# Kernel optimization log

Measured on AMD Instinct MI355X. Metric: run time of the kernel, lower is better.

The kernel has to match this reference:

```python
import jax, jax.numpy as jnp
import numpy as np

TOP_K = 2

def setup_inputs() -> dict:
    key = jax.random.key(0)
    ks = jax.random.split(key, 6)
    B, L, D, E = 4, 4096, 1024, 8
    s = 1.0 / np.sqrt(D)
    return {
        "x": jax.random.normal(ks[0], (B, L, D), dtype=jnp.float32),
        "Wr": jax.random.normal(ks[1], (E, D), dtype=jnp.float32) * s,
        "W1": jax.random.normal(ks[2], (E, D, D), dtype=jnp.float32) * s,
        "b1": jax.random.normal(ks[3], (E, D), dtype=jnp.float32) * 0.01,
        "W2": jax.random.normal(ks[4], (E, D, D), dtype=jnp.float32) * s,
        "b2": jax.random.normal(ks[5], (E, D), dtype=jnp.float32) * 0.01,
    }

def reference(x, Wr, W1, b1, W2, b2):
    # x: [B,L,D]; Wr: [E,D]; W1/W2: [E,D,D]; b1/b2: [E,D]
    E = Wr.shape[0]
    logits = jnp.einsum("bld,ed->ble", x, Wr)           # router, no bias
    probs = jax.nn.softmax(logits, axis=-1)
    topw, topi = jax.lax.top_k(probs, TOP_K)             # [B,L,K]
    topw = topw / jnp.sum(topw, axis=-1, keepdims=True)  # renormalize
    # combine weights per expert: [B,L,E], zero where expert not selected
    comb = jnp.sum(jax.nn.one_hot(topi, E, dtype=x.dtype) * topw[..., None], axis=-2)
    out = jnp.zeros_like(x)
    for e in range(E):  # small fixed expert count
        h = jax.nn.gelu(jnp.einsum("bld,fd->blf", x, W1[e]) + b1[e], approximate=False)
        y = jnp.einsum("blf,df->bld", h, W2[e]) + b2[e]
        out = out + comb[..., e:e + 1] * y
    return out
```

## Files before the change

### kernel.cpp

```cpp
#include <hip/hip_runtime.h>
#include <hip/hip_bf16.h>
#include <cstdint>
#include <cstddef>

#define NTOK 16384
#define DDIM 1024
#define NEXP 8
#define CPAD 32

typedef __attribute__((ext_vector_type(8))) short bf16x8;
typedef __attribute__((ext_vector_type(4))) float f32x4;

__device__ __forceinline__ unsigned short f2bf(float f) {
  union { float f; unsigned u; } c; c.f = f;
  unsigned r = (c.u + 0x7FFFu + ((c.u >> 16) & 1u)) >> 16;
  return (unsigned short)r;
}

__device__ __forceinline__ float gelu_exact(float v) {
  return 0.5f * v * (1.0f + erff(v * 0.70710678118654752440f));
}

#define GL2LDS(gp, lp) __builtin_amdgcn_global_load_lds( \
    (__attribute__((address_space(1))) void*)(gp),       \
    (__attribute__((address_space(3))) void*)(lp), 16, 0, 0)

__global__ void cast_k(const float* __restrict__ src, unsigned short* __restrict__ dst, int n4) {
  int i = blockIdx.x * blockDim.x + threadIdx.x;
  if (i >= n4) return;
  float4 a = ((const float4*)src)[i];
  union { unsigned short s[4]; uint2 v; } o;
  o.s[0] = f2bf(a.x); o.s[1] = f2bf(a.y); o.s[2] = f2bf(a.z); o.s[3] = f2bf(a.w);
  ((uint2*)dst)[i] = o.v;
}

__global__ __launch_bounds__(256)
void castx_router_k(const float* __restrict__ x, const float* __restrict__ Wr,
                    unsigned short* __restrict__ xb, int* __restrict__ tokE,
                    float2* __restrict__ tokW) {
  const int t = blockIdx.x;
  const int tid = threadIdx.x;
  const int w = tid >> 6, lane = tid & 63;

  float4 xv = ((const float4*)x)[(size_t)t * 256 + tid];
  union { unsigned short s[4]; uint2 v; } o;
  o.s[0] = f2bf(xv.x); o.s[1] = f2bf(xv.y); o.s[2] = f2bf(xv.z); o.s[3] = f2bf(xv.w);
  ((uint2*)xb)[(size_t)t * 256 + tid] = o.v;

  const float4* Wr4 = (const float4*)Wr;
  float p[NEXP];
#pragma unroll
  for (int e = 0; e < NEXP; ++e) {
    float4 wv = Wr4[e * 256 + tid];
    p[e] = xv.x * wv.x + xv.y * wv.y + xv.z * wv.z + xv.w * wv.w;
  }
#pragma unroll
  for (int e = 0; e < NEXP; ++e) {
    float v = p[e];
#pragma unroll
    for (int off = 32; off >= 1; off >>= 1) v += __shfl_xor(v, off, 64);
    p[e] = v;
  }
  __shared__ float red[4][NEXP];
  if (lane == 0) {
#pragma unroll
    for (int e = 0; e < NEXP; ++e) red[w][e] = p[e];
  }
  __syncthreads();
  if (tid == 0) {
    float s[NEXP];
#pragma unroll
    for (int e = 0; e < NEXP; ++e) s[e] = red[0][e] + red[1][e] + red[2][e] + red[3][e];
    int e1 = 0; float m1 = s[0];
#pragma unroll
    for (int e = 1; e < NEXP; ++e) if (s[e] > m1) { m1 = s[e]; e1 = e; }
    int e2 = -1; float m2 = -3.4e38f;
#pragma unroll
    for (int e = 0; e < NEXP; ++e) {
      if (e == e1) continue;
      if (s[e] > m2) { m2 = s[e]; e2 = e; }
    }
    float dd = expf(m2 - m1);
    tokE[t] = e1 | (e2 << 8);
    tokW[t] = make_float2(1.f / (1.f + dd), dd / (1.f + dd));
  }
}

__global__ __launch_bounds__(256)
void hist_k(const int* __restrict__ tokE, int* __restrict__ cnt) {
  const int t = blockIdx.x * blockDim.x + threadIdx.x;
  const int w = threadIdx.x >> 6, lane = threadIdx.x & 63;
  const int pk = tokE[t];
  const int e1 = pk & 0xFF, e2 = (pk >> 8) & 0xFF;
  __shared__ int h[4][NEXP];
#pragma unroll
  for (int e = 0; e < NEXP; ++e) {
    int c = (int)__popcll(__ballot(e1 == e)) + (int)__popcll(__ballot(e2 == e));
    if (lane == 0) h[w][e] = c;
  }
  __syncthreads();
  if (threadIdx.x < NEXP) {
    int tot = h[0][threadIdx.x] + h[1][threadIdx.x] + h[2][threadIdx.x] + h[3][threadIdx.x];
    atomicAdd(&cnt[threadIdx.x * CPAD], tot);
  }
}

__global__ void offsets_k(const int* __restrict__ cnt, int* __restrict__ off) {
  if (threadIdx.x == 0) {
    int a = 0;
    for (int e = 0; e < NEXP; ++e) { off[e] = a; a += cnt[e * CPAD]; }
  }
}

__device__ __forceinline__ int bucket_slot(int* cur, int e_sel) {
  int lane = threadIdx.x & 63;
  int slot = 0;
#pragma unroll
  for (int e = 0; e < NEXP; ++e) {
    unsigned long long m = __ballot(e_sel == e);
    if (e_sel == e) {
      unsigned long long below = m & ((1ull << lane) - 1ull);
      int leader = __ffsll((long long)m) - 1;
      int base = 0;
      if (lane == leader) base = atomicAdd(&cur[e * CPAD], (int)__popcll(m));
      base = __shfl(base, leader, 64);
      slot = base + (int)__popcll(below);
    }
  }
  return slot;
}

__global__ __launch_bounds__(256)
void place_k(const int* __restrict__ tokE, const float2* __restrict__ tokW,
             const int* __restrict__ off, int* __restrict__ cur,
             int* __restrict__ asgT, float* __restrict__ asgW) {
  int t = blockIdx.x * blockDim.x + threadIdx.x;
  if (t >= NTOK) return;
  int pk = tokE[t];
  float2 w = tokW[t];
  int e1 = pk & 0xFF, e2 = (pk >> 8) & 0xFF;
  int p1 = off[e1] + bucket_slot(cur, e1);
  asgT[p1] = t; asgW[p1] = w.x;
  int p2 = off[e2] + bucket_slot(cur, e2);
  asgT[p2] = t; asgW[p2] = w.y;
}

__global__ __launch_bounds__(256)
void gemm1_k(const unsigned short* __restrict__ xb, const unsigned short* __restrict__ w1b,
             const float* __restrict__ b1, const int* __restrict__ cntp,
             const int* __restrict__ offp, const int* __restrict__ asgT,
             unsigned short* __restrict__ h) {
  const int e = blockIdx.z;
  const int cnt = cntp[e * CPAD];
  const int m0 = blockIdx.x * 128;
  if (m0 >= cnt) return;
  const int off = offp[e];
  const int n0 = blockIdx.y * 128;

  __shared__ __align__(16) unsigned short As[2][4096];
  __shared__ __align__(16) unsigned short Bs[2][4096];

  const int tid = threadIdx.x;
  const int w = tid >> 6, lane = tid & 63;
  const int r = lane & 15, kc = lane >> 4;

  const unsigned short* srcA[2];
  const unsigned short* srcB[2];
#pragma unroll
  for (int j = 0; j < 2; ++j) {
    int g = j * 4 + w;
    int rowt = m0 + g * 16 + r;
    int rowc = (rowt < cnt) ? rowt : m0;
    int tok = asgT[off + rowc];
    srcA[j] = xb + (size_t)tok * DDIM + kc * 8;
    int coln = n0 + g * 16 + r;
    srcB[j] = w1b + (size_t)e * DDIM * DDIM + (size_t)coln * DDIM + kc * 8;
  }

  f32x4 acc[4][4];
#pragma unroll
  for (int i = 0; i < 4; ++i)
#pragma unroll
    for (int j = 0; j < 4; ++j) acc[i][j] = (f32x4){0.f, 0.f, 0.f, 0.f};

  auto stage = [&](int buf, int k0) {
#pragma unroll
    for (int j = 0; j < 2; ++j) {
      int g = j * 4 + w;
      GL2LDS(srcA[j] + k0, &As[buf][g * 512 + lane * 8]);
      GL2LDS(srcB[j] + k0, &Bs[buf][g * 512 + lane * 8]);
    }
  };

  const int wr = w >> 1, wc = w & 1;
  stage(0, 0);
#pragma unroll 2
  for (int s = 0; s < 32; ++s) {
    int buf = s & 1;
    __syncthreads();
    if (s + 1 < 32) stage(buf ^ 1, (s + 1) * 32);
    bf16x8 af[4], bv[4];
#pragma unroll
    for (int i = 0; i < 4; ++i) {
      af[i] = *(const bf16x8*)&As[buf][(wr * 4 + i) * 512 + lane * 8];
      bv[i] = *(const bf16x8*)&Bs[buf][(wc * 4 + i) * 512 + lane * 8];
    }
#pragma unroll
    for (int i = 0; i < 4; ++i)
#pragma unroll
      for (int j = 0; j < 4; ++j)
        acc[i][j] = __builtin_amdgcn_mfma_f32_16x16x32_bf16(af[i], bv[j], acc[i][j], 0, 0, 0);
  }

  float bcol[4];
#pragma unroll
  for (int j = 0; j < 4; ++j) bcol[j] = b1[e * DDIM + n0 + wc * 64 + j * 16 + r];
#pragma unroll
  for (int i = 0; i < 4; ++i) {
#pragma unroll
    for (int q = 0; q < 4; ++q) {
      int grow = m0 + wr * 64 + i * 16 + kc * 4 + q;
      if (grow < cnt) {
        size_t hrow = (size_t)(off + grow) * DDIM;
#pragma unroll
        for (int j = 0; j < 4; ++j) {
          int col = n0 + wc * 64 + j * 16 + r;
          h[hrow + col] = f2bf(gelu_exact(acc[i][j][q] + bcol[j]));
        }
      }
    }
  }
}

__global__ __launch_bounds__(256)
void gemm2_k(const unsigned short* __restrict__ hsrc, const unsigned short* __restrict__ w2b,
             const float* __restrict__ b2, const int* __restrict__ cntp,
             const int* __restrict__ offp, const int* __restrict__ asgT,
             const float* __restrict__ asgW, float* __restrict__ out) {
  const int e = blockIdx.z;
  const int cnt = cntp[e * CPAD];
  const int m0 = blockIdx.x * 128;
  if (m0 >= cnt) return;
  const int off = offp[e];
  const int n0 = blockIdx.y * 128;

  __shared__ __align__(16) unsigned short As[2][4096];
  __shared__ __align__(16) unsigned short Bs[2][4096];

  const int tid = threadIdx.x;
  const int w = tid >> 6, lane = tid & 63;
  const int r = lane & 15, kc = lane >> 4;

  const unsigned short* srcA[2];
  const unsigned short* srcB[2];
#pragma unroll
  for (int j = 0; j < 2; ++j) {
    int g = j * 4 + w;
    int rowt = m0 + g * 16 + r;
    int rowc = (rowt < cnt) ? rowt : m0;
    srcA[j] = hsrc + (size_t)(off + rowc) * DDIM + kc * 8;
    int coln = n0 + g * 16 + r;
    srcB[j] = w2b + (size_t)e * DDIM * DDIM + (size_t)coln * DDIM + kc * 8;
  }

  f32x4 acc[4][4];
#pragma unroll
  for (int i = 0; i < 4; ++i)
#pragma unroll
    for (int j = 0; j < 4; ++j) acc[i][j] = (f32x4){0.f, 0.f, 0.f, 0.f};

  auto stage = [&](int buf, int k0) {
#pragma unroll
    for (int j = 0; j < 2; ++j) {
      int g = j * 4 + w;
      GL2LDS(srcA[j] + k0, &As[buf][g * 512 + lane * 8]);
      GL2LDS(srcB[j] + k0, &Bs[buf][g * 512 + lane * 8]);
    }
  };

  const int wr = w >> 1, wc = w & 1;
  stage(0, 0);
#pragma unroll 2
  for (int s = 0; s < 32; ++s) {
    int buf = s & 1;
    __syncthreads();
    if (s + 1 < 32) stage(buf ^ 1, (s + 1) * 32);
    bf16x8 af[4], bv[4];
#pragma unroll
    for (int i = 0; i < 4; ++i) {
      af[i] = *(const bf16x8*)&As[buf][(wr * 4 + i) * 512 + lane * 8];
      bv[i] = *(const bf16x8*)&Bs[buf][(wc * 4 + i) * 512 + lane * 8];
    }
#pragma unroll
    for (int i = 0; i < 4; ++i)
#pragma unroll
      for (int j = 0; j < 4; ++j)
        acc[i][j] = __builtin_amdgcn_mfma_f32_16x16x32_bf16(af[i], bv[j], acc[i][j], 0, 0, 0);
  }

  float bcol[4];
#pragma unroll
  for (int j = 0; j < 4; ++j) bcol[j] = b2[e * DDIM + n0 + wc * 64 + j * 16 + r];
#pragma unroll
  for (int i = 0; i < 4; ++i) {
#pragma unroll
    for (int q = 0; q < 4; ++q) {
      int grow = m0 + wr * 64 + i * 16 + kc * 4 + q;
      if (grow < cnt) {
        int tok = asgT[off + grow];
        float wgt = asgW[off + grow];
        float* orow = out + (size_t)tok * DDIM;
#pragma unroll
        for (int j = 0; j < 4; ++j) {
          int col = n0 + wc * 64 + j * 16 + r;
          atomicAdd(&orow[col], wgt * (acc[i][j][q] + bcol[j]));
        }
      }
    }
  }
}

extern "C" void kernel_launch(void* const* d_in, const int* in_sizes, int n_in,
                              void* d_out, int out_size, void* d_ws, size_t ws_size,
                              hipStream_t stream) {
  (void)in_sizes; (void)n_in; (void)ws_size;
  const float* x  = (const float*)d_in[0];
  const float* Wr = (const float*)d_in[1];
  const float* W1 = (const float*)d_in[2];
  const float* b1 = (const float*)d_in[3];
  const float* W2 = (const float*)d_in[4];
  const float* b2 = (const float*)d_in[5];
  float* out = (float*)d_out;

  char* ws = (char*)d_ws;
  int*    cnt  = (int*)(ws + 0);
  int*    off  = (int*)(ws + 4096);
  int*    cur  = (int*)(ws + 8192);
  int*    tokE = (int*)(ws + 16384);
  float2* tokW = (float2*)(ws + 16384 + 65536);
  int*    asgT = (int*)(ws + 16384 + 65536 + 131072);
  float*  asgW = (float*)(ws + 16384 + 65536 + 131072 + 131072);
  unsigned short* xb  = (unsigned short*)(ws + (size_t)(1u << 20));
  unsigned short* w1b = (unsigned short*)(ws + (size_t)33 * (1u << 20));
  unsigned short* w2b = (unsigned short*)(ws + (size_t)49 * (1u << 20));
  unsigned short* h   = (unsigned short*)(ws + (size_t)65 * (1u << 20));

  hipMemsetAsync(ws, 0, 16384, stream);
  hipMemsetAsync(d_out, 0, (size_t)out_size * sizeof(float), stream);

  const int nW = NEXP * DDIM * DDIM;
  cast_k<<<(nW / 4) / 256, 256, 0, stream>>>(W1, w1b, nW / 4);
  cast_k<<<(nW / 4) / 256, 256, 0, stream>>>(W2, w2b, nW / 4);

  castx_router_k<<<NTOK, 256, 0, stream>>>(x, Wr, xb, tokE, tokW);
  hist_k<<<NTOK / 256, 256, 0, stream>>>(tokE, cnt);
  offsets_k<<<1, 64, 0, stream>>>(cnt, off);
  place_k<<<NTOK / 256, 256, 0, stream>>>(tokE, tokW, off, cur, asgT, asgW);

  dim3 ggrid(128, 8, NEXP);
  gemm1_k<<<ggrid, 256, 0, stream>>>(xb, w1b, b1, cnt, off, asgT, h);
  gemm2_k<<<ggrid, 256, 0, stream>>>(h, w2b, b2, cnt, off, asgT, asgW, out);
}
```

Measured before the change: 742.0 us.

## Enlarge expert GEMM tiles to 256x256 with 8 waves and K-step 64

```diff
diff --git a/kernel.cpp b/kernel.cpp
--- a/kernel.cpp
+++ b/kernel.cpp
@@ -145,81 +145,88 @@
   asgT[p2] = t; asgW[p2] = w.y;
 }
 
-__global__ __launch_bounds__(256)
+
+__global__ __launch_bounds__(512, 2)
 void gemm1_k(const unsigned short* __restrict__ xb, const unsigned short* __restrict__ w1b,
              const float* __restrict__ b1, const int* __restrict__ cntp,
              const int* __restrict__ offp, const int* __restrict__ asgT,
              unsigned short* __restrict__ h) {
   const int e = blockIdx.z;
   const int cnt = cntp[e * CPAD];
-  const int m0 = blockIdx.x * 128;
+  const int m0 = blockIdx.x * 256;
   if (m0 >= cnt) return;
   const int off = offp[e];
-  const int n0 = blockIdx.y * 128;
-
-  __shared__ __align__(16) unsigned short As[2][4096];
-  __shared__ __align__(16) unsigned short Bs[2][4096];
+  const int n0 = blockIdx.y * 256;
+
+  __shared__ __align__(16) unsigned short As[2][16384];
+  __shared__ __align__(16) unsigned short Bs[2][16384];
 
   const int tid = threadIdx.x;
   const int w = tid >> 6, lane = tid & 63;
   const int r = lane & 15, kc = lane >> 4;
+  const int wr = w >> 2, wc = w & 3;
 
   const unsigned short* srcA[2];
   const unsigned short* srcB[2];
 #pragma unroll
-  for (int j = 0; j < 2; ++j) {
-    int g = j * 4 + w;
+  for (int i = 0; i < 2; ++i) {
+    int g = 2 * w + i;
     int rowt = m0 + g * 16 + r;
     int rowc = (rowt < cnt) ? rowt : m0;
     int tok = asgT[off + rowc];
-    srcA[j] = xb + (size_t)tok * DDIM + kc * 8;
+    srcA[i] = xb + (size_t)tok * DDIM + kc * 8;
     int coln = n0 + g * 16 + r;
-    srcB[j] = w1b + (size_t)e * DDIM * DDIM + (size_t)coln * DDIM + kc * 8;
-  }
-
-  f32x4 acc[4][4];
-#pragma unroll
-  for (int i = 0; i < 4; ++i)
+    srcB[i] = w1b + (size_t)e * DDIM * DDIM + (size_t)coln * DDIM + kc * 8;
+  }
+
+  f32x4 acc[8][4];
+#pragma unroll
+  for (int i = 0; i < 8; ++i)
 #pragma unroll
     for (int j = 0; j < 4; ++j) acc[i][j] = (f32x4){0.f, 0.f, 0.f, 0.f};
 
   auto stage = [&](int buf, int k0) {
 #pragma unroll
-    for (int j = 0; j < 2; ++j) {
-      int g = j * 4 + w;
-      GL2LDS(srcA[j] + k0, &As[buf][g * 512 + lane * 8]);
-      GL2LDS(srcB[j] + k0, &Bs[buf][g * 512 + lane * 8]);
+    for (int i = 0; i < 2; ++i) {
+      int g = 2 * w + i;
+#pragma unroll
+      for (int ks = 0; ks < 2; ++ks) {
+        GL2LDS(srcA[i] + k0 + ks * 32, &As[buf][g * 1024 + ks * 512 + lane * 8]);
+        GL2LDS(srcB[i] + k0 + ks * 32, &Bs[buf][g * 1024 + ks * 512 + lane * 8]);
+      }
     }
   };
 
-  const int wr = w >> 1, wc = w & 1;
   stage(0, 0);
-#pragma unroll 2
-  for (int s = 0; s < 32; ++s) {
+  for (int s = 0; s < 16; ++s) {
     int buf = s & 1;
     __syncthreads();
-    if (s + 1 < 32) stage(buf ^ 1, (s + 1) * 32);
-    bf16x8 af[4], bv[4];
-#pragma unroll
-    for (int i = 0; i < 4; ++i) {
-      af[i] = *(const bf16x8*)&As[buf][(wr * 4 + i) * 512 + lane * 8];
-      bv[i] = *(const bf16x8*)&Bs[buf][(wc * 4 + i) * 512 + lane * 8];
-    }
-#pragma unroll
-    for (int i = 0; i < 4; ++i)
+    if (s + 1 < 16) stage(buf ^ 1, (s + 1) * 64);
+#pragma unroll
+    for (int ks = 0; ks < 2; ++ks) {
+      bf16x8 af[8], bv[4];
+#pragma unroll
+      for (int i = 0; i < 8; ++i)
+        af[i] = *(const bf16x8*)&As[buf][(wr * 8 + i) * 1024 + ks * 512 + lane * 8];
 #pragma unroll
       for (int j = 0; j < 4; ++j)
-        acc[i][j] = __builtin_amdgcn_mfma_f32_16x16x32_bf16(af[i], bv[j], acc[i][j], 0, 0, 0);
+        bv[j] = *(const bf16x8*)&Bs[buf][(wc * 4 + j) * 1024 + ks * 512 + lane * 8];
+#pragma unroll
+      for (int i = 0; i < 8; ++i)
+#pragma unroll
+        for (int j = 0; j < 4; ++j)
+          acc[i][j] = __builtin_amdgcn_mfma_f32_16x16x32_bf16(af[i], bv[j], acc[i][j], 0, 0, 0);
+    }
   }
 
   float bcol[4];
 #pragma unroll
   for (int j = 0; j < 4; ++j) bcol[j] = b1[e * DDIM + n0 + wc * 64 + j * 16 + r];
 #pragma unroll
-  for (int i = 0; i < 4; ++i) {
+  for (int i = 0; i < 8; ++i) {
 #pragma unroll
     for (int q = 0; q < 4; ++q) {
-      int grow = m0 + wr * 64 + i * 16 + kc * 4 + q;
+      int grow = m0 + wr * 128 + i * 16 + kc * 4 + q;
       if (grow < cnt) {
         size_t hrow = (size_t)(off + grow) * DDIM;
 #pragma unroll
@@ -232,80 +239,86 @@
   }
 }
 
-__global__ __launch_bounds__(256)
+__global__ __launch_bounds__(512, 2)
 void gemm2_k(const unsigned short* __restrict__ hsrc, const unsigned short* __restrict__ w2b,
              const float* __restrict__ b2, const int* __restrict__ cntp,
              const int* __restrict__ offp, const int* __restrict__ asgT,
              const float* __restrict__ asgW, float* __restrict__ out) {
   const int e = blockIdx.z;
   const int cnt = cntp[e * CPAD];
-  const int m0 = blockIdx.x * 128;
+  const int m0 = blockIdx.x * 256;
   if (m0 >= cnt) return;
   const int off = offp[e];
-  const int n0 = blockIdx.y * 128;
-
-  __shared__ __align__(16) unsigned short As[2][4096];
-  __shared__ __align__(16) unsigned short Bs[2][4096];
+  const int n0 = blockIdx.y * 256;
+
+  __shared__ __align__(16) unsigned short As[2][16384];
+  __shared__ __align__(16) unsigned short Bs[2][16384];
 
   const int tid = threadIdx.x;
   const int w = tid >> 6, lane = tid & 63;
   const int r = lane & 15, kc = lane >> 4;
+  const int wr = w >> 2, wc = w & 3;
 
   const unsigned short* srcA[2];
   const unsigned short* srcB[2];
 #pragma unroll
-  for (int j = 0; j < 2; ++j) {
-    int g = j * 4 + w;
+  for (int i = 0; i < 2; ++i) {
+    int g = 2 * w + i;
     int rowt = m0 + g * 16 + r;
     int rowc = (rowt < cnt) ? rowt : m0;
-    srcA[j] = hsrc + (size_t)(off + rowc) * DDIM + kc * 8;
+    srcA[i] = hsrc + (size_t)(off + rowc) * DDIM + kc * 8;
     int coln = n0 + g * 16 + r;
-    srcB[j] = w2b + (size_t)e * DDIM * DDIM + (size_t)coln * DDIM + kc * 8;
-  }
-
-  f32x4 acc[4][4];
-#pragma unroll
-  for (int i = 0; i < 4; ++i)
+    srcB[i] = w2b + (size_t)e * DDIM * DDIM + (size_t)coln * DDIM + kc * 8;
+  }
+
+  f32x4 acc[8][4];
+#pragma unroll
+  for (int i = 0; i < 8; ++i)
 #pragma unroll
     for (int j = 0; j < 4; ++j) acc[i][j] = (f32x4){0.f, 0.f, 0.f, 0.f};
 
   auto stage = [&](int buf, int k0) {
 #pragma unroll
-    for (int j = 0; j < 2; ++j) {
-      int g = j * 4 + w;
-      GL2LDS(srcA[j] + k0, &As[buf][g * 512 + lane * 8]);
-      GL2LDS(srcB[j] + k0, &Bs[buf][g * 512 + lane * 8]);
+    for (int i = 0; i < 2; ++i) {
+      int g = 2 * w + i;
+#pragma unroll
+      for (int ks = 0; ks < 2; ++ks) {
+        GL2LDS(srcA[i] + k0 + ks * 32, &As[buf][g * 1024 + ks * 512 + lane * 8]);
+        GL2LDS(srcB[i] + k0 + ks * 32, &Bs[buf][g * 1024 + ks * 512 + lane * 8]);
+      }
     }
   };
 
-  const int wr = w >> 1, wc = w & 1;
   stage(0, 0);
-#pragma unroll 2
-  for (int s = 0; s < 32; ++s) {
+  for (int s = 0; s < 16; ++s) {
     int buf = s & 1;
     __syncthreads();
-    if (s + 1 < 32) stage(buf ^ 1, (s + 1) * 32);
-    bf16x8 af[4], bv[4];
-#pragma unroll
-    for (int i = 0; i < 4; ++i) {
-      af[i] = *(const bf16x8*)&As[buf][(wr * 4 + i) * 512 + lane * 8];
-      bv[i] = *(const bf16x8*)&Bs[buf][(wc * 4 + i) * 512 + lane * 8];
-    }
-#pragma unroll
-    for (int i = 0; i < 4; ++i)
+    if (s + 1 < 16) stage(buf ^ 1, (s + 1) * 64);
+#pragma unroll
+    for (int ks = 0; ks < 2; ++ks) {
+      bf16x8 af[8], bv[4];
+#pragma unroll
+      for (int i = 0; i < 8; ++i)
+        af[i] = *(const bf16x8*)&As[buf][(wr * 8 + i) * 1024 + ks * 512 + lane * 8];
 #pragma unroll
       for (int j = 0; j < 4; ++j)
-        acc[i][j] = __builtin_amdgcn_mfma_f32_16x16x32_bf16(af[i], bv[j], acc[i][j], 0, 0, 0);
+        bv[j] = *(const bf16x8*)&Bs[buf][(wc * 4 + j) * 1024 + ks * 512 + lane * 8];
+#pragma unroll
+      for (int i = 0; i < 8; ++i)
+#pragma unroll
+        for (int j = 0; j < 4; ++j)
+          acc[i][j] = __builtin_amdgcn_mfma_f32_16x16x32_bf16(af[i], bv[j], acc[i][j], 0, 0, 0);
+    }
   }
 
   float bcol[4];
 #pragma unroll
   for (int j = 0; j < 4; ++j) bcol[j] = b2[e * DDIM + n0 + wc * 64 + j * 16 + r];
 #pragma unroll
-  for (int i = 0; i < 4; ++i) {
+  for (int i = 0; i < 8; ++i) {
 #pragma unroll
     for (int q = 0; q < 4; ++q) {
-      int grow = m0 + wr * 64 + i * 16 + kc * 4 + q;
+      int grow = m0 + wr * 128 + i * 16 + kc * 4 + q;
       if (grow < cnt) {
         int tok = asgT[off + grow];
         float wgt = asgW[off + grow];
@@ -357,7 +370,7 @@
   offsets_k<<<1, 64, 0, stream>>>(cnt, off);
   place_k<<<NTOK / 256, 256, 0, stream>>>(tokE, tokW, off, cur, asgT, asgW);
 
-  dim3 ggrid(128, 8, NEXP);
-  gemm1_k<<<ggrid, 256, 0, stream>>>(xb, w1b, b1, cnt, off, asgT, h);
-  gemm2_k<<<ggrid, 256, 0, stream>>>(h, w2b, b2, cnt, off, asgT, asgW, out);
-}
+  dim3 ggrid(64, 4, NEXP);
+  gemm1_k<<<ggrid, 512, 0, stream>>>(xb, w1b, b1, cnt, off, asgT, h);
+  gemm2_k<<<ggrid, 512, 0, stream>>>(h, w2b, b2, cnt, off, asgT, asgW, out);
+}
```

Measured after the change: 715.4 us. -3.6%, faster.

## Triple-buffer LDS staging with explicit vmcnt waits in expert GEMMs

Applied to the files above, without the earlier changes.

```diff
diff --git a/kernel.cpp b/kernel.cpp
--- a/kernel.cpp
+++ b/kernel.cpp
@@ -145,7 +145,8 @@
   asgT[p2] = t; asgW[p2] = w.y;
 }
 
-__global__ __launch_bounds__(256)
+
+__global__ __launch_bounds__(256, 3)
 void gemm1_k(const unsigned short* __restrict__ xb, const unsigned short* __restrict__ w1b,
              const float* __restrict__ b1, const int* __restrict__ cntp,
              const int* __restrict__ offp, const int* __restrict__ asgT,
@@ -157,24 +158,25 @@
   const int off = offp[e];
   const int n0 = blockIdx.y * 128;
 
-  __shared__ __align__(16) unsigned short As[2][4096];
-  __shared__ __align__(16) unsigned short Bs[2][4096];
+  __shared__ __align__(16) unsigned short As[3][4096];
+  __shared__ __align__(16) unsigned short Bs[3][4096];
 
   const int tid = threadIdx.x;
   const int w = tid >> 6, lane = tid & 63;
   const int r = lane & 15, kc = lane >> 4;
+  const int wr = w >> 1, wc = w & 1;
 
   const unsigned short* srcA[2];
   const unsigned short* srcB[2];
 #pragma unroll
-  for (int j = 0; j < 2; ++j) {
-    int g = j * 4 + w;
+  for (int i = 0; i < 2; ++i) {
+    int g = w + i * 4;
     int rowt = m0 + g * 16 + r;
     int rowc = (rowt < cnt) ? rowt : m0;
     int tok = asgT[off + rowc];
-    srcA[j] = xb + (size_t)tok * DDIM + kc * 8;
+    srcA[i] = xb + (size_t)tok * DDIM + kc * 8;
     int coln = n0 + g * 16 + r;
-    srcB[j] = w1b + (size_t)e * DDIM * DDIM + (size_t)coln * DDIM + kc * 8;
+    srcB[i] = w1b + (size_t)e * DDIM * DDIM + (size_t)coln * DDIM + kc * 8;
   }
 
   f32x4 acc[4][4];
@@ -185,31 +187,38 @@
 
   auto stage = [&](int buf, int k0) {
 #pragma unroll
-    for (int j = 0; j < 2; ++j) {
-      int g = j * 4 + w;
-      GL2LDS(srcA[j] + k0, &As[buf][g * 512 + lane * 8]);
-      GL2LDS(srcB[j] + k0, &Bs[buf][g * 512 + lane * 8]);
+    for (int i = 0; i < 2; ++i) {
+      int g = w + i * 4;
+      GL2LDS(srcA[i] + k0, &As[buf][g * 512 + lane * 8]);
+      GL2LDS(srcB[i] + k0, &Bs[buf][g * 512 + lane * 8]);
     }
   };
 
-  const int wr = w >> 1, wc = w & 1;
   stage(0, 0);
-#pragma unroll 2
-  for (int s = 0; s < 32; ++s) {
-    int buf = s & 1;
-    __syncthreads();
-    if (s + 1 < 32) stage(buf ^ 1, (s + 1) * 32);
+  stage(1, 32);
+  int bc = 0;
+  for (int t = 0; t < 32; ++t) {
+    if (t < 31) asm volatile("s_waitcnt vmcnt(4)" ::: "memory");
+    else        asm volatile("s_waitcnt vmcnt(0)" ::: "memory");
+    __builtin_amdgcn_sched_barrier(0);
+    __builtin_amdgcn_s_barrier();
+    __builtin_amdgcn_sched_barrier(0);
+    if (t + 2 < 32) {
+      int bs = bc + 2; if (bs >= 3) bs -= 3;
+      stage(bs, (t + 2) * 32);
+    }
     bf16x8 af[4], bv[4];
 #pragma unroll
     for (int i = 0; i < 4; ++i) {
-      af[i] = *(const bf16x8*)&As[buf][(wr * 4 + i) * 512 + lane * 8];
-      bv[i] = *(const bf16x8*)&Bs[buf][(wc * 4 + i) * 512 + lane * 8];
+      af[i] = *(const bf16x8*)&As[bc][(wr * 4 + i) * 512 + lane * 8];
+      bv[i] = *(const bf16x8*)&Bs[bc][(wc * 4 + i) * 512 + lane * 8];
     }
 #pragma unroll
     for (int i = 0; i < 4; ++i)
 #pragma unroll
       for (int j = 0; j < 4; ++j)
         acc[i][j] = __builtin_amdgcn_mfma_f32_16x16x32_bf16(af[i], bv[j], acc[i][j], 0, 0, 0);
+    bc = (bc == 2) ? 0 : bc + 1;
   }
 
   float bcol[4];
@@ -232,7 +241,7 @@
   }
 }
 
-__global__ __launch_bounds__(256)
+__global__ __launch_bounds__(256, 3)
 void gemm2_k(const unsigned short* __restrict__ hsrc, const unsigned short* __restrict__ w2b,
              const float* __restrict__ b2, const int* __restrict__ cntp,
              const int* __restrict__ offp, const int* __restrict__ asgT,
@@ -244,23 +253,24 @@
   const int off = offp[e];
   const int n0 = blockIdx.y * 128;
 
-  __shared__ __align__(16) unsigned short As[2][4096];
-  __shared__ __align__(16) unsigned short Bs[2][4096];
+  __shared__ __align__(16) unsigned short As[3][4096];
+  __shared__ __align__(16) unsigned short Bs[3][4096];
 
   const int tid = threadIdx.x;
   const int w = tid >> 6, lane = tid & 63;
   const int r = lane & 15, kc = lane >> 4;
+  const int wr = w >> 1, wc = w & 1;
 
   const unsigned short* srcA[2];
   const unsigned short* srcB[2];
 #pragma unroll
-  for (int j = 0; j < 2; ++j) {
-    int g = j * 4 + w;
+  for (int i = 0; i < 2; ++i) {
+    int g = w + i * 4;
     int rowt = m0 + g * 16 + r;
     int rowc = (rowt < cnt) ? rowt : m0;
-    srcA[j] = hsrc + (size_t)(off + rowc) * DDIM + kc * 8;
+    srcA[i] = hsrc + (size_t)(off + rowc) * DDIM + kc * 8;
     int coln = n0 + g * 16 + r;
-    srcB[j] = w2b + (size_t)e * DDIM * DDIM + (size_t)coln * DDIM + kc * 8;
+    srcB[i] = w2b + (size_t)e * DDIM * DDIM + (size_t)coln * DDIM + kc * 8;
   }
 
   f32x4 acc[4][4];
@@ -271,31 +281,38 @@
 
   auto stage = [&](int buf, int k0) {
 #pragma unroll
-    for (int j = 0; j < 2; ++j) {
-      int g = j * 4 + w;
-      GL2LDS(srcA[j] + k0, &As[buf][g * 512 + lane * 8]);
-      GL2LDS(srcB[j] + k0, &Bs[buf][g * 512 + lane * 8]);
+    for (int i = 0; i < 2; ++i) {
+      int g = w + i * 4;
+      GL2LDS(srcA[i] + k0, &As[buf][g * 512 + lane * 8]);
+      GL2LDS(srcB[i] + k0, &Bs[buf][g * 512 + lane * 8]);
     }
   };
 
-  const int wr = w >> 1, wc = w & 1;
   stage(0, 0);
-#pragma unroll 2
-  for (int s = 0; s < 32; ++s) {
-    int buf = s & 1;
-    __syncthreads();
-    if (s + 1 < 32) stage(buf ^ 1, (s + 1) * 32);
+  stage(1, 32);
+  int bc = 0;
+  for (int t = 0; t < 32; ++t) {
+    if (t < 31) asm volatile("s_waitcnt vmcnt(4)" ::: "memory");
+    else        asm volatile("s_waitcnt vmcnt(0)" ::: "memory");
+    __builtin_amdgcn_sched_barrier(0);
+    __builtin_amdgcn_s_barrier();
+    __builtin_amdgcn_sched_barrier(0);
+    if (t + 2 < 32) {
+      int bs = bc + 2; if (bs >= 3) bs -= 3;
+      stage(bs, (t + 2) * 32);
+    }
     bf16x8 af[4], bv[4];
 #pragma unroll
     for (int i = 0; i < 4; ++i) {
-      af[i] = *(const bf16x8*)&As[buf][(wr * 4 + i) * 512 + lane * 8];
-      bv[i] = *(const bf16x8*)&Bs[buf][(wc * 4 + i) * 512 + lane * 8];
+      af[i] = *(const bf16x8*)&As[bc][(wr * 4 + i) * 512 + lane * 8];
+      bv[i] = *(const bf16x8*)&Bs[bc][(wc * 4 + i) * 512 + lane * 8];
     }
 #pragma unroll
     for (int i = 0; i < 4; ++i)
 #pragma unroll
       for (int j = 0; j < 4; ++j)
         acc[i][j] = __builtin_amdgcn_mfma_f32_16x16x32_bf16(af[i], bv[j], acc[i][j], 0, 0, 0);
+    bc = (bc == 2) ? 0 : bc + 1;
   }
 
   float bcol[4];
```

New measurement: 701.3 us. 5.5% less time.

## Group tokens by expert pair and fuse second GEMM over both experts

Applied to the files above, without the earlier changes.

```diff
diff --git a/kernel.cpp b/kernel.cpp
--- a/kernel.cpp
+++ b/kernel.cpp
@@ -6,6 +6,7 @@
 #define NTOK 16384
 #define DDIM 1024
 #define NEXP 8
+#define NPAIR 64
 #define CPAD 32
 
 typedef __attribute__((ext_vector_type(8))) short bf16x8;
@@ -25,26 +26,30 @@
     (__attribute__((address_space(1))) void*)(gp),       \
     (__attribute__((address_space(3))) void*)(lp), 16, 0, 0)
 
-__global__ void cast_k(const float* __restrict__ src, unsigned short* __restrict__ dst, int n4) {
+__global__ void castw_k(const float* __restrict__ W1, const float* __restrict__ W2,
+                        unsigned short* __restrict__ w1b, unsigned short* __restrict__ w2b) {
+  const int H = 2 * 1024 * 1024;
   int i = blockIdx.x * blockDim.x + threadIdx.x;
-  if (i >= n4) return;
-  float4 a = ((const float4*)src)[i];
-  union { unsigned short s[4]; uint2 v; } o;
-  o.s[0] = f2bf(a.x); o.s[1] = f2bf(a.y); o.s[2] = f2bf(a.z); o.s[3] = f2bf(a.w);
-  ((uint2*)dst)[i] = o.v;
+  const float4* s; unsigned short* d; int k;
+  if (i < H) { s = (const float4*)W1; d = w1b; k = i; }
+  else       { s = (const float4*)W2; d = w2b; k = i - H; }
+  float4 a = s[k];
+  union { unsigned short s4[4]; uint2 v; } o;
+  o.s4[0] = f2bf(a.x); o.s4[1] = f2bf(a.y); o.s4[2] = f2bf(a.z); o.s4[3] = f2bf(a.w);
+  ((uint2*)d)[k] = o.v;
 }
 
 __global__ __launch_bounds__(256)
 void castx_router_k(const float* __restrict__ x, const float* __restrict__ Wr,
-                    unsigned short* __restrict__ xb, int* __restrict__ tokE,
+                    unsigned short* __restrict__ xb, int* __restrict__ tokP,
                     float2* __restrict__ tokW) {
   const int t = blockIdx.x;
   const int tid = threadIdx.x;
   const int w = tid >> 6, lane = tid & 63;
 
   float4 xv = ((const float4*)x)[(size_t)t * 256 + tid];
-  union { unsigned short s[4]; uint2 v; } o;
-  o.s[0] = f2bf(xv.x); o.s[1] = f2bf(xv.y); o.s[2] = f2bf(xv.z); o.s[3] = f2bf(xv.w);
+  union { unsigned short s4[4]; uint2 v; } o;
+  o.s4[0] = f2bf(xv.x); o.s4[1] = f2bf(xv.y); o.s4[2] = f2bf(xv.z); o.s4[3] = f2bf(xv.w);
   ((uint2*)xb)[(size_t)t * 256 + tid] = o.v;
 
   const float4* Wr4 = (const float4*)Wr;
@@ -81,81 +86,86 @@
       if (s[e] > m2) { m2 = s[e]; e2 = e; }
     }
     float dd = expf(m2 - m1);
-    tokE[t] = e1 | (e2 << 8);
-    tokW[t] = make_float2(1.f / (1.f + dd), dd / (1.f + dd));
-  }
-}
-
-__global__ __launch_bounds__(256)
-void hist_k(const int* __restrict__ tokE, int* __restrict__ cnt) {
-  const int t = blockIdx.x * blockDim.x + threadIdx.x;
-  const int w = threadIdx.x >> 6, lane = threadIdx.x & 63;
-  const int pk = tokE[t];
-  const int e1 = pk & 0xFF, e2 = (pk >> 8) & 0xFF;
-  __shared__ int h[4][NEXP];
-#pragma unroll
-  for (int e = 0; e < NEXP; ++e) {
-    int c = (int)__popcll(__ballot(e1 == e)) + (int)__popcll(__ballot(e2 == e));
-    if (lane == 0) h[w][e] = c;
-  }
+    float w1 = 1.f / (1.f + dd);
+    float w2 = dd / (1.f + dd);
+    int lo = e1 < e2 ? e1 : e2;
+    int hi = e1 < e2 ? e2 : e1;
+    float wlo = (e1 < e2) ? w1 : w2;
+    float whi = (e1 < e2) ? w2 : w1;
+    tokP[t] = lo * 8 + hi;
+    tokW[t] = make_float2(wlo, whi);
+  }
+}
+
+__global__ __launch_bounds__(256)
+void hist_k(const int* __restrict__ tokP, int* __restrict__ cnt) {
+  __shared__ int bins[NPAIR];
+  if (threadIdx.x < NPAIR) bins[threadIdx.x] = 0;
   __syncthreads();
-  if (threadIdx.x < NEXP) {
-    int tot = h[0][threadIdx.x] + h[1][threadIdx.x] + h[2][threadIdx.x] + h[3][threadIdx.x];
-    atomicAdd(&cnt[threadIdx.x * CPAD], tot);
-  }
-}
-
-__global__ void offsets_k(const int* __restrict__ cnt, int* __restrict__ off) {
+  int t = blockIdx.x * 256 + threadIdx.x;
+  atomicAdd(&bins[tokP[t]], 1);
+  __syncthreads();
+  if (threadIdx.x < NPAIR) {
+    int c = bins[threadIdx.x];
+    if (c) atomicAdd(&cnt[threadIdx.x * CPAD], c);
+  }
+}
+
+__global__ void offsets_k(const int* __restrict__ cnt, int* __restrict__ off,
+                          int* __restrict__ map, int* __restrict__ nwork) {
   if (threadIdx.x == 0) {
-    int a = 0;
-    for (int e = 0; e < NEXP; ++e) { off[e] = a; a += cnt[e * CPAD]; }
-  }
-}
-
-__device__ __forceinline__ int bucket_slot(int* cur, int e_sel) {
+    int a = 0, nw = 0;
+    for (int s = 0; s < NPAIR; ++s) {
+      off[s] = a;
+      int c = cnt[s * CPAD];
+      a += c;
+      for (int mt = 0; mt * 128 < c; ++mt) map[nw++] = (s << 16) | mt;
+    }
+    nwork[0] = nw;
+  }
+}
+
+__global__ __launch_bounds__(256)
+void place_k(const int* __restrict__ tokP, const float2* __restrict__ tokW,
+             const int* __restrict__ off, int* __restrict__ cur,
+             int* __restrict__ asgT, float2* __restrict__ asgW2) {
+  int t = blockIdx.x * 256 + threadIdx.x;
+  int pid = tokP[t];
   int lane = threadIdx.x & 63;
   int slot = 0;
-#pragma unroll
-  for (int e = 0; e < NEXP; ++e) {
-    unsigned long long m = __ballot(e_sel == e);
-    if (e_sel == e) {
-      unsigned long long below = m & ((1ull << lane) - 1ull);
+#pragma unroll 1
+  for (int s = 0; s < NPAIR; ++s) {
+    unsigned long long m = __ballot(pid == s);
+    if (pid == s) {
       int leader = __ffsll((long long)m) - 1;
       int base = 0;
-      if (lane == leader) base = atomicAdd(&cur[e * CPAD], (int)__popcll(m));
+      if (lane == leader) base = atomicAdd(&cur[s * CPAD], (int)__popcll(m));
       base = __shfl(base, leader, 64);
-      slot = base + (int)__popcll(below);
-    }
-  }
-  return slot;
-}
-
-__global__ __launch_bounds__(256)
-void place_k(const int* __restrict__ tokE, const float2* __restrict__ tokW,
-             const int* __restrict__ off, int* __restrict__ cur,
-             int* __restrict__ asgT, float* __restrict__ asgW) {
-  int t = blockIdx.x * blockDim.x + threadIdx.x;
-  if (t >= NTOK) return;
-  int pk = tokE[t];
-  float2 w = tokW[t];
-  int e1 = pk & 0xFF, e2 = (pk >> 8) & 0xFF;
-  int p1 = off[e1] + bucket_slot(cur, e1);
-  asgT[p1] = t; asgW[p1] = w.x;
-  int p2 = off[e2] + bucket_slot(cur, e2);
-  asgT[p2] = t; asgW[p2] = w.y;
-}
+      slot = base + (int)__popcll(m & ((1ull << lane) - 1ull));
+    }
+  }
+  int p = off[pid] + slot;
+  asgT[p] = t;
+  asgW2[p] = tokW[t];
+}
+
 
 __global__ __launch_bounds__(256)
 void gemm1_k(const unsigned short* __restrict__ xb, const unsigned short* __restrict__ w1b,
              const float* __restrict__ b1, const int* __restrict__ cntp,
-             const int* __restrict__ offp, const int* __restrict__ asgT,
-             unsigned short* __restrict__ h) {
-  const int e = blockIdx.z;
-  const int cnt = cntp[e * CPAD];
-  const int m0 = blockIdx.x * 128;
-  if (m0 >= cnt) return;
-  const int off = offp[e];
+             const int* __restrict__ offp, const int* __restrict__ map,
+             const int* __restrict__ nwork, const int* __restrict__ asgT,
+             const float2* __restrict__ asgW2, unsigned short* __restrict__ h) {
+  if ((int)blockIdx.x >= nwork[0]) return;
+  const int mp = map[blockIdx.x];
+  const int pid = mp >> 16, mt = mp & 0xFFFF;
+  const int cnt = cntp[pid * CPAD];
+  const int off = offp[pid];
+  const int m0 = mt * 128;
   const int n0 = blockIdx.y * 128;
+  const int half = n0 >> 10;
+  const int e = half ? (pid & 7) : (pid >> 3);
+  const int nc0 = n0 & 1023;
 
   __shared__ __align__(16) unsigned short As[2][4096];
   __shared__ __align__(16) unsigned short Bs[2][4096];
@@ -163,18 +173,19 @@
   const int tid = threadIdx.x;
   const int w = tid >> 6, lane = tid & 63;
   const int r = lane & 15, kc = lane >> 4;
+  const int wr = w >> 1, wc = w & 1;
 
   const unsigned short* srcA[2];
   const unsigned short* srcB[2];
 #pragma unroll
-  for (int j = 0; j < 2; ++j) {
-    int g = j * 4 + w;
+  for (int i = 0; i < 2; ++i) {
+    int g = w + i * 4;
     int rowt = m0 + g * 16 + r;
     int rowc = (rowt < cnt) ? rowt : m0;
     int tok = asgT[off + rowc];
-    srcA[j] = xb + (size_t)tok * DDIM + kc * 8;
-    int coln = n0 + g * 16 + r;
-    srcB[j] = w1b + (size_t)e * DDIM * DDIM + (size_t)coln * DDIM + kc * 8;
+    srcA[i] = xb + (size_t)tok * DDIM + kc * 8;
+    int coln = nc0 + g * 16 + r;
+    srcB[i] = w1b + (size_t)e * DDIM * DDIM + (size_t)coln * DDIM + kc * 8;
   }
 
   f32x4 acc[4][4];
@@ -185,20 +196,19 @@
 
   auto stage = [&](int buf, int k0) {
 #pragma unroll
-    for (int j = 0; j < 2; ++j) {
-      int g = j * 4 + w;
-      GL2LDS(srcA[j] + k0, &As[buf][g * 512 + lane * 8]);
-      GL2LDS(srcB[j] + k0, &Bs[buf][g * 512 + lane * 8]);
+    for (int i = 0; i < 2; ++i) {
+      int g = w + i * 4;
+      GL2LDS(srcA[i] + k0, &As[buf][g * 512 + lane * 8]);
+      GL2LDS(srcB[i] + k0, &Bs[buf][g * 512 + lane * 8]);
     }
   };
 
-  const int wr = w >> 1, wc = w & 1;
   stage(0, 0);
 #pragma unroll 2
-  for (int s = 0; s < 32; ++s) {
-    int buf = s & 1;
+  for (int t = 0; t < 32; ++t) {
+    int buf = t & 1;
     __syncthreads();
-    if (s + 1 < 32) stage(buf ^ 1, (s + 1) * 32);
+    if (t + 1 < 32) stage(buf ^ 1, (t + 1) * 32);
     bf16x8 af[4], bv[4];
 #pragma unroll
     for (int i = 0; i < 4; ++i) {
@@ -214,18 +224,20 @@
 
   float bcol[4];
 #pragma unroll
-  for (int j = 0; j < 4; ++j) bcol[j] = b1[e * DDIM + n0 + wc * 64 + j * 16 + r];
+  for (int j = 0; j < 4; ++j) bcol[j] = b1[e * DDIM + nc0 + wc * 64 + j * 16 + r];
 #pragma unroll
   for (int i = 0; i < 4; ++i) {
 #pragma unroll
     for (int q = 0; q < 4; ++q) {
       int grow = m0 + wr * 64 + i * 16 + kc * 4 + q;
       if (grow < cnt) {
-        size_t hrow = (size_t)(off + grow) * DDIM;
+        float2 wv = asgW2[off + grow];
+        float sc = half ? wv.y : wv.x;
+        size_t hrow = (size_t)(off + grow) * 2048;
 #pragma unroll
         for (int j = 0; j < 4; ++j) {
           int col = n0 + wc * 64 + j * 16 + r;
-          h[hrow + col] = f2bf(gelu_exact(acc[i][j][q] + bcol[j]));
+          h[hrow + col] = f2bf(sc * gelu_exact(acc[i][j][q] + bcol[j]));
         }
       }
     }
@@ -235,32 +247,38 @@
 __global__ __launch_bounds__(256)
 void gemm2_k(const unsigned short* __restrict__ hsrc, const unsigned short* __restrict__ w2b,
              const float* __restrict__ b2, const int* __restrict__ cntp,
-             const int* __restrict__ offp, const int* __restrict__ asgT,
-             const float* __restrict__ asgW, float* __restrict__ out) {
-  const int e = blockIdx.z;
-  const int cnt = cntp[e * CPAD];
-  const int m0 = blockIdx.x * 128;
-  if (m0 >= cnt) return;
-  const int off = offp[e];
+             const int* __restrict__ offp, const int* __restrict__ map,
+             const int* __restrict__ nwork, const int* __restrict__ asgT,
+             const float2* __restrict__ asgW2, float* __restrict__ out) {
+  if ((int)blockIdx.x >= nwork[0]) return;
+  const int mp = map[blockIdx.x];
+  const int pid = mp >> 16, mt = mp & 0xFFFF;
+  const int cnt = cntp[pid * CPAD];
+  const int off = offp[pid];
+  const int m0 = mt * 128;
   const int n0 = blockIdx.y * 128;
-
-  __shared__ __align__(16) unsigned short As[2][4096];
-  __shared__ __align__(16) unsigned short Bs[2][4096];
+  const int elo = pid >> 3, ehi = pid & 7;
+
+  __shared__ __align__(16) unsigned short As[2][8192];
+  __shared__ __align__(16) unsigned short Bs[2][8192];
 
   const int tid = threadIdx.x;
   const int w = tid >> 6, lane = tid & 63;
   const int r = lane & 15, kc = lane >> 4;
+  const int wr = w >> 1, wc = w & 1;
 
   const unsigned short* srcA[2];
-  const unsigned short* srcB[2];
-#pragma unroll
-  for (int j = 0; j < 2; ++j) {
-    int g = j * 4 + w;
+  const unsigned short* srcBlo[2];
+  const unsigned short* srcBhi[2];
+#pragma unroll
+  for (int i = 0; i < 2; ++i) {
+    int g = w + i * 4;
     int rowt = m0 + g * 16 + r;
     int rowc = (rowt < cnt) ? rowt : m0;
-    srcA[j] = hsrc + (size_t)(off + rowc) * DDIM + kc * 8;
+    srcA[i] = hsrc + (size_t)(off + rowc) * 2048 + kc * 8;
     int coln = n0 + g * 16 + r;
-    srcB[j] = w2b + (size_t)e * DDIM * DDIM + (size_t)coln * DDIM + kc * 8;
+    srcBlo[i] = w2b + (size_t)elo * DDIM * DDIM + (size_t)coln * DDIM + kc * 8;
+    srcBhi[i] = w2b + (size_t)ehi * DDIM * DDIM + (size_t)coln * DDIM + kc * 8;
   }
 
   f32x4 acc[4][4];
@@ -270,37 +288,47 @@
     for (int j = 0; j < 4; ++j) acc[i][j] = (f32x4){0.f, 0.f, 0.f, 0.f};
 
   auto stage = [&](int buf, int k0) {
-#pragma unroll
-    for (int j = 0; j < 2; ++j) {
-      int g = j * 4 + w;
-      GL2LDS(srcA[j] + k0, &As[buf][g * 512 + lane * 8]);
-      GL2LDS(srcB[j] + k0, &Bs[buf][g * 512 + lane * 8]);
+    int kb = k0 & 1023;
+#pragma unroll
+    for (int i = 0; i < 2; ++i) {
+      int g = w + i * 4;
+      const unsigned short* pb = (k0 & 1024) ? srcBhi[i] : srcBlo[i];
+#pragma unroll
+      for (int ks = 0; ks < 2; ++ks) {
+        GL2LDS(srcA[i] + k0 + ks * 32, &As[buf][(g * 2 + ks) * 512 + lane * 8]);
+        GL2LDS(pb + kb + ks * 32,      &Bs[buf][(g * 2 + ks) * 512 + lane * 8]);
+      }
     }
   };
 
-  const int wr = w >> 1, wc = w & 1;
   stage(0, 0);
-#pragma unroll 2
-  for (int s = 0; s < 32; ++s) {
-    int buf = s & 1;
+  for (int t = 0; t < 32; ++t) {
+    int buf = t & 1;
     __syncthreads();
-    if (s + 1 < 32) stage(buf ^ 1, (s + 1) * 32);
-    bf16x8 af[4], bv[4];
-#pragma unroll
-    for (int i = 0; i < 4; ++i) {
-      af[i] = *(const bf16x8*)&As[buf][(wr * 4 + i) * 512 + lane * 8];
-      bv[i] = *(const bf16x8*)&Bs[buf][(wc * 4 + i) * 512 + lane * 8];
-    }
-#pragma unroll
-    for (int i = 0; i < 4; ++i)
-#pragma unroll
-      for (int j = 0; j < 4; ++j)
-        acc[i][j] = __builtin_amdgcn_mfma_f32_16x16x32_bf16(af[i], bv[j], acc[i][j], 0, 0, 0);
-  }
-
-  float bcol[4];
-#pragma unroll
-  for (int j = 0; j < 4; ++j) bcol[j] = b2[e * DDIM + n0 + wc * 64 + j * 16 + r];
+    if (t + 1 < 32) stage(buf ^ 1, (t + 1) * 64);
+#pragma unroll
+    for (int ks = 0; ks < 2; ++ks) {
+      bf16x8 af[4], bv[4];
+#pragma unroll
+      for (int i = 0; i < 4; ++i) {
+        af[i] = *(const bf16x8*)&As[buf][((wr * 4 + i) * 2 + ks) * 512 + lane * 8];
+        bv[i] = *(const bf16x8*)&Bs[buf][((wc * 4 + i) * 2 + ks) * 512 + lane * 8];
+      }
+#pragma unroll
+      for (int i = 0; i < 4; ++i)
+#pragma unroll
+        for (int j = 0; j < 4; ++j)
+          acc[i][j] = __builtin_amdgcn_mfma_f32_16x16x32_bf16(af[i], bv[j], acc[i][j], 0, 0, 0);
+    }
+  }
+
+  float b2lo[4], b2hi[4];
+#pragma unroll
+  for (int j = 0; j < 4; ++j) {
+    int col = n0 + wc * 64 + j * 16 + r;
+    b2lo[j] = b2[elo * DDIM + col];
+    b2hi[j] = b2[ehi * DDIM + col];
+  }
 #pragma unroll
   for (int i = 0; i < 4; ++i) {
 #pragma unroll
@@ -308,12 +336,12 @@
       int grow = m0 + wr * 64 + i * 16 + kc * 4 + q;
       if (grow < cnt) {
         int tok = asgT[off + grow];
-        float wgt = asgW[off + grow];
+        float2 wv = asgW2[off + grow];
         float* orow = out + (size_t)tok * DDIM;
 #pragma unroll
         for (int j = 0; j < 4; ++j) {
           int col = n0 + wc * 64 + j * 16 + r;
-          atomicAdd(&orow[col], wgt * (acc[i][j][q] + bcol[j]));
+          orow[col] = acc[i][j][q] + wv.x * b2lo[j] + wv.y * b2hi[j];
         }
       }
     }
@@ -323,7 +351,7 @@
 extern "C" void kernel_launch(void* const* d_in, const int* in_sizes, int n_in,
                               void* d_out, int out_size, void* d_ws, size_t ws_size,
                               hipStream_t stream) {
-  (void)in_sizes; (void)n_in; (void)ws_size;
+  (void)in_sizes; (void)n_in; (void)ws_size; (void)out_size;
   const float* x  = (const float*)d_in[0];
   const float* Wr = (const float*)d_in[1];
   const float* W1 = (const float*)d_in[2];
@@ -333,31 +361,30 @@
   float* out = (float*)d_out;
 
   char* ws = (char*)d_ws;
-  int*    cnt  = (int*)(ws + 0);
-  int*    off  = (int*)(ws + 4096);
-  int*    cur  = (int*)(ws + 8192);
-  int*    tokE = (int*)(ws + 16384);
-  float2* tokW = (float2*)(ws + 16384 + 65536);
-  int*    asgT = (int*)(ws + 16384 + 65536 + 131072);
-  float*  asgW = (float*)(ws + 16384 + 65536 + 131072 + 131072);
+  int*    cnt   = (int*)(ws + 0);
+  int*    cur   = (int*)(ws + 8192);
+  int*    off   = (int*)(ws + 16384);
+  int*    nwork = (int*)(ws + 16640);
+  int*    map   = (int*)(ws + 16648);
+  int*    tokP  = (int*)(ws + 32768);
+  float2* tokW  = (float2*)(ws + 98304);
+  int*    asgT  = (int*)(ws + 229376);
+  float2* asgW2 = (float2*)(ws + 294912);
   unsigned short* xb  = (unsigned short*)(ws + (size_t)(1u << 20));
   unsigned short* w1b = (unsigned short*)(ws + (size_t)33 * (1u << 20));
   unsigned short* w2b = (unsigned short*)(ws + (size_t)49 * (1u << 20));
   unsigned short* h   = (unsigned short*)(ws + (size_t)65 * (1u << 20));
 
   hipMemsetAsync(ws, 0, 16384, stream);
-  hipMemsetAsync(d_out, 0, (size_t)out_size * sizeof(float), stream);
-
-  const int nW = NEXP * DDIM * DDIM;
-  cast_k<<<(nW / 4) / 256, 256, 0, stream>>>(W1, w1b, nW / 4);
-  cast_k<<<(nW / 4) / 256, 256, 0, stream>>>(W2, w2b, nW / 4);
-
-  castx_router_k<<<NTOK, 256, 0, stream>>>(x, Wr, xb, tokE, tokW);
-  hist_k<<<NTOK / 256, 256, 0, stream>>>(tokE, cnt);
-  offsets_k<<<1, 64, 0, stream>>>(cnt, off);
-  place_k<<<NTOK / 256, 256, 0, stream>>>(tokE, tokW, off, cur, asgT, asgW);
-
-  dim3 ggrid(128, 8, NEXP);
-  gemm1_k<<<ggrid, 256, 0, stream>>>(xb, w1b, b1, cnt, off, asgT, h);
-  gemm2_k<<<ggrid, 256, 0, stream>>>(h, w2b, b2, cnt, off, asgT, asgW, out);
-}
+
+  castw_k<<<16384, 256, 0, stream>>>(W1, W2, w1b, w2b);
+  castx_router_k<<<NTOK, 256, 0, stream>>>(x, Wr, xb, tokP, tokW);
+  hist_k<<<NTOK / 256, 256, 0, stream>>>(tokP, cnt);
+  offsets_k<<<1, 64, 0, stream>>>(cnt, off, map, nwork);
+  place_k<<<NTOK / 256, 256, 0, stream>>>(tokP, tokW, off, cur, asgT, asgW2);
+
+  dim3 g1(160, 16);
+  dim3 g2(160, 8);
+  gemm1_k<<<g1, 256, 0, stream>>>(xb, w1b, b1, cnt, off, map, nwork, asgT, asgW2, h);
+  gemm2_k<<<g2, 256, 0, stream>>>(h, w2b, b2, cnt, off, map, nwork, asgT, asgW2, out);
+}
```

After: 682.5 us. 8.0% less time.
